# Kernel tuning notes

Measured on AMD Instinct MI355X. Metric: run time of the kernel, lower is better.

The kernel has to match this reference:

```python
import jax, jax.numpy as jnp
import numpy as np

N, F, H, C = 50000, 128, 4, 32  # nodes, in-features, heads, per-head dim
E = 800000
D = H * C  # concat output dim = 128


def _tconv(x, src, dst, ea, Wq, bq, Wk, bk, Wv, bv, We, Ws, bs):
    # PyG TransformerConv (concat=True, root_weight=True, beta=False, eval mode)
    n = x.shape[0]
    q = (x @ Wq + bq).reshape(n, H, C)
    k = (x @ Wk + bk).reshape(n, H, C)
    v = (x @ Wv + bv).reshape(n, H, C)
    e = (ea @ We).reshape(-1, H, C)            # edge embedding [E,H,C]
    kj = k[src] + e                            # gathered keys + edge emb
    alpha = jnp.einsum('ehc,ehc->eh', q[dst], kj) / jnp.sqrt(jnp.float32(C))
    amax = jax.ops.segment_max(alpha, dst, num_segments=n)
    ex = jnp.exp(alpha - amax[dst])
    denom = jax.ops.segment_sum(ex, dst, num_segments=n)
    w = ex / (denom[dst] + 1e-16)              # segment softmax over in-edges
    msg = (v[src] + e) * w[:, :, None]
    out = jax.ops.segment_sum(msg, dst, num_segments=n).reshape(n, D)
    return out + x @ Ws + bs                   # skip connection


def setup_inputs() -> dict:
    key = jax.random.key(0)
    ks = jax.random.split(key, 24)
    s = lambda i, shape, scale: jax.random.normal(ks[i], shape, dtype=jnp.float32) * scale
    inp = {
        'x': s(0, (N, F), 1.0),
        'edge_index': jax.random.randint(ks[1], (2, E), 0, N),
        'edge_attr': s(2, (E,), 1.0),
        # layer 1 (in = F)
        'Wq1': s(3, (F, D), 1.0 / np.sqrt(F)), 'bq1': jnp.zeros((D,), jnp.float32),
        'Wk1': s(4, (F, D), 1.0 / np.sqrt(F)), 'bk1': jnp.zeros((D,), jnp.float32),
        'Wv1': s(5, (F, D), 1.0 / np.sqrt(F)), 'bv1': jnp.zeros((D,), jnp.float32),
        'We1': s(6, (1, D), 1.0),
        'Ws1': s(7, (F, D), 1.0 / np.sqrt(F)), 'bs1': jnp.zeros((D,), jnp.float32),
        # layer 2 (in = D)
        'Wq2': s(8, (D, D), 1.0 / np.sqrt(D)), 'bq2': jnp.zeros((D,), jnp.float32),
        'Wk2': s(9, (D, D), 1.0 / np.sqrt(D)), 'bk2': jnp.zeros((D,), jnp.float32),
        'Wv2': s(10, (D, D), 1.0 / np.sqrt(D)), 'bv2': jnp.zeros((D,), jnp.float32),
        'We2': s(11, (1, D), 1.0),
        'Ws2': s(12, (D, D), 1.0 / np.sqrt(D)), 'bs2': jnp.zeros((D,), jnp.float32),
    }
    return inp


def reference(x, edge_index, edge_attr,
              Wq1, bq1, Wk1, bk1, Wv1, bv1, We1, Ws1, bs1,
              Wq2, bq2, Wk2, bk2, Wv2, bv2, We2, Ws2, bs2):
    src, dst = edge_index[0], edge_index[1]
    ea = edge_attr.reshape(-1, 1)
    h = _tconv(x, src, dst, ea, Wq1, bq1, Wk1, bk1, Wv1, bv1, We1, Ws1, bs1)
    h = jax.nn.relu(h)  # dropout is identity in eval mode
    h = _tconv(h, src, dst, ea, Wq2, bq2, Wk2, bk2, Wv2, bv2, We2, Ws2, bs2)
    return jax.nn.relu(h)
```

## Files before the change

### kernel.cpp

```cpp
#include <hip/hip_runtime.h>


#define TPB 256

typedef __attribute__((ext_vector_type(8))) short short8v;
typedef __attribute__((ext_vector_type(8))) unsigned short ushort8v;
typedef __attribute__((ext_vector_type(16))) float f32x16;

__device__ __forceinline__ unsigned short f2bf(float f) {
    unsigned u = __float_as_uint(f);
    u = (u + 0x7FFFu + ((u >> 16) & 1u)) >> 16;
    return (unsigned short)u;
}
__device__ __forceinline__ float bf2f(unsigned short s) {
    return __uint_as_float((unsigned)s << 16);
}
__device__ __forceinline__ float exp2_hw(float x) {
    float r;
    asm("v_exp_f32 %0, %1" : "=v"(r) : "v"(x));
    return r;
}

__device__ __forceinline__ void gemm_body(
    int idx, int nrt,
    const unsigned short* __restrict__ A, int M,
    const unsigned short* __restrict__ pack,
    const float* __restrict__ bq, const float* __restrict__ bk,
    const float* __restrict__ bv, const float* __restrict__ bs,
    unsigned short* __restrict__ oq, unsigned short* __restrict__ okv,
    unsigned short* __restrict__ os)
{
    if (idx >= nrt * 4) return;
    const int g = idx & 3;
    const int row0 = (idx >> 2) * 128;

    const int wv = threadIdx.x >> 6;
    const int lane = threadIdx.x & 63;
    const int rbase = row0 + wv * 32;
    const int arow = rbase + (lane & 31);
    const int kh = (lane >> 5) * 8;

    const short8v z8 = {0, 0, 0, 0, 0, 0, 0, 0};
    short8v a[8];
    if (arow < M) {
        const unsigned short* Ap = A + (size_t)arow * 128 + kh;
#pragma unroll
        for (int t = 0; t < 8; ++t) a[t] = *(const short8v*)(Ap + t * 16);
    } else {
#pragma unroll
        for (int t = 0; t < 8; ++t) a[t] = z8;
    }

    f32x16 acc[4];
#pragma unroll
    for (int nc = 0; nc < 4; ++nc)
#pragma unroll
        for (int r = 0; r < 16; ++r) acc[nc][r] = 0.f;

    const unsigned short* bp = pack + (size_t)g * 16384;
#pragma unroll
    for (int nc = 0; nc < 4; ++nc) {
#pragma unroll
        for (int t = 0; t < 8; ++t) {
            short8v b = *(const short8v*)(bp + (nc * 8 + t) * 512 + lane * 8);
            acc[nc] = __builtin_amdgcn_mfma_f32_32x32x16_bf16(a[t], b, acc[nc], 0, 0, 0);
        }
    }

    const float* bias = g == 0 ? bq : (g == 1 ? bk : (g == 2 ? bv : bs));
    const int col = lane & 31;
    const int rb2 = rbase + 4 * (lane >> 5);
    unsigned short* out = g == 0 ? oq : (g == 3 ? os : okv);
    const int stride = (g == 1 || g == 2) ? 256 : 128;
    const int goff = g == 2 ? 128 : 0;
#pragma unroll
    for (int nc = 0; nc < 4; ++nc) {
        float bb = bias[nc * 32 + col];
#pragma unroll
        for (int r = 0; r < 16; ++r) {
            int row = rb2 + (r & 3) + 8 * (r >> 2);
            if (row < M)
                out[(size_t)row * stride + goff + nc * 32 + col] = f2bf(acc[nc][r] + bb);
        }
    }
}

__device__ __forceinline__ void scatter_body(
    int sb, const int* __restrict__ src, const int* __restrict__ dst,
    const float* __restrict__ ea, const int* __restrict__ row_ptr,
    const int* __restrict__ edge_rank,
    unsigned* __restrict__ csr_pack, int E)
{
    const int base = (sb * TPB + threadIdx.x) * 4;
    if (base + 3 < E) {
        int4 d4 = *(const int4*)(dst + base);
        int4 s4 = *(const int4*)(src + base);
        float4 a4 = *(const float4*)(ea + base);
        int4 r4 = *(const int4*)(edge_rank + base);
        csr_pack[row_ptr[d4.x] + r4.x] = ((unsigned)f2bf(a4.x) << 16) | (unsigned)s4.x;
        csr_pack[row_ptr[d4.y] + r4.y] = ((unsigned)f2bf(a4.y) << 16) | (unsigned)s4.y;
        csr_pack[row_ptr[d4.z] + r4.z] = ((unsigned)f2bf(a4.z) << 16) | (unsigned)s4.z;
        csr_pack[row_ptr[d4.w] + r4.w] = ((unsigned)f2bf(a4.w) << 16) | (unsigned)s4.w;
    } else {
        for (int e = base; e < E; ++e) {
            csr_pack[row_ptr[dst[e]] + edge_rank[e]] =
                ((unsigned)f2bf(ea[e]) << 16) | (unsigned)src[e];
        }
    }
}

__global__ void __launch_bounds__(TPB) hist_prep_cvt_k(
    const int* __restrict__ dst, int* __restrict__ deg,
    int* __restrict__ edge_rank, int E, int gE4,
    const float* __restrict__ Wq1, const float* __restrict__ Wk1,
    const float* __restrict__ Wv1, const float* __restrict__ Ws1,
    const float* __restrict__ Wq2, const float* __restrict__ Wk2,
    const float* __restrict__ Wv2, const float* __restrict__ Ws2,
    unsigned short* __restrict__ pack,
    const float* __restrict__ x, unsigned short* __restrict__ xb, int n4)
{
    if (blockIdx.x < (unsigned)gE4) {
        const int base = (blockIdx.x * TPB + threadIdx.x) * 4;
        if (base + 3 < E) {
            int4 d4 = *(const int4*)(dst + base);
            int4 r4;
            r4.x = atomicAdd(&deg[d4.x], 1);
            r4.y = atomicAdd(&deg[d4.y], 1);
            r4.z = atomicAdd(&deg[d4.z], 1);
            r4.w = atomicAdd(&deg[d4.w], 1);
            *(int4*)(edge_rank + base) = r4;
        } else {
            for (int e = base; e < E; ++e)
                edge_rank[e] = atomicAdd(&deg[dst[e]], 1);
        }
    } else if (blockIdx.x < (unsigned)(gE4 + 512)) {
        int i = (blockIdx.x - gE4) * TPB + threadIdx.x;
        int j = i & 7, lane = (i >> 3) & 63, t = (i >> 9) & 7, nc = (i >> 12) & 3, g = (i >> 14) & 7;
        const float* Wt[8] = {Wq1, Wk1, Wv1, Ws1, Wq2, Wk2, Wv2, Ws2};
        const float* W = Wt[g];
        int kk = t * 16 + (lane >> 5) * 8 + j;
        int nn = nc * 32 + (lane & 31);
        pack[i] = f2bf(W[kk * 128 + nn]);
    } else {
        int i = (blockIdx.x - gE4 - 512) * TPB + threadIdx.x;
        if (i >= n4) return;
        float4 v = *(const float4*)(x + (size_t)i * 4);
        ushort4 o;
        o.x = f2bf(v.x); o.y = f2bf(v.y); o.z = f2bf(v.z); o.w = f2bf(v.w);
        *(ushort4*)(xb + (size_t)i * 4) = o;
    }
}

__global__ void __launch_bounds__(TPB) scan_a_k(const int* __restrict__ deg, int n,
                                                int* __restrict__ incl,
                                                int* __restrict__ bsum,
                                                int* __restrict__ bcnt, int nb,
                                                int* __restrict__ rank)
{
    __shared__ int ts[TPB];
    __shared__ int lhist[64];
    if (threadIdx.x < 64) lhist[threadIdx.x] = 0;
    const int base = blockIdx.x * 1024;
    int vals[4], s = 0;
#pragma unroll
    for (int j = 0; j < 4; ++j) {
        int i = base + threadIdx.x * 4 + j;
        vals[j] = (i < n) ? deg[i] : 0;
        s += vals[j];
    }
    ts[threadIdx.x] = s;
    __syncthreads();
#pragma unroll
    for (int j = 0; j < 4; ++j) {
        int i = base + threadIdx.x * 4 + j;
        if (i < n) {
            int bin = 63 - min(vals[j], 63);
            rank[i] = atomicAdd(&lhist[bin], 1);
        }
    }
    for (int off = 1; off < TPB; off <<= 1) {
        int u = (threadIdx.x >= off) ? ts[threadIdx.x - off] : 0;
        __syncthreads();
        ts[threadIdx.x] += u;
        __syncthreads();
    }
    int run = ts[threadIdx.x] - s;
#pragma unroll
    for (int j = 0; j < 4; ++j) {
        run += vals[j];
        int i = base + threadIdx.x * 4 + j;
        if (i < n) incl[i] = run;
    }
    if (threadIdx.x == TPB - 1) bsum[blockIdx.x] = ts[TPB - 1];
    __syncthreads();
    if (threadIdx.x < 64) bcnt[threadIdx.x * nb + blockIdx.x] = lhist[threadIdx.x];
}

__global__ void __launch_bounds__(TPB) scan_b_k(int* __restrict__ bsum, int nb,
                                                int* __restrict__ bcnt)
{
    __shared__ int ts[TPB];
    const int t = threadIdx.x;
    int v = (t < nb) ? bsum[t] : 0;
    ts[t] = v;
    __syncthreads();
    for (int off = 1; off < TPB; off <<= 1) {
        int u = (t >= off) ? ts[t - off] : 0;
        __syncthreads();
        ts[t] += u;
        __syncthreads();
    }
    if (t < nb) bsum[t] = ts[t] - v;
    __syncthreads();

    const int total = 64 * nb;
    const int C = (total + TPB - 1) / TPB;
    int loc[32];
    int s = 0;
    for (int j = 0; j < C; ++j) {
        int i = t * C + j;
        loc[j] = (i < total) ? bcnt[i] : 0;
        s += loc[j];
    }
    __syncthreads();
    ts[t] = s;
    __syncthreads();
    for (int off = 1; off < TPB; off <<= 1) {
        int u = (t >= off) ? ts[t - off] : 0;
        __syncthreads();
        ts[t] += u;
        __syncthreads();
    }
    int run = ts[t] - s;
    for (int j = 0; j < C; ++j) {
        int i = t * C + j;
        if (i < total) bcnt[i] = run;
        run += loc[j];
    }
}

__global__ void __launch_bounds__(TPB) finalize_k(const int* __restrict__ incl,
                                                  const int* __restrict__ deg,
                                                  const int* __restrict__ bsum, int n,
                                                  int* __restrict__ row_ptr,
                                                  const int* __restrict__ bcnt, int nb,
                                                  const int* __restrict__ rank,
                                                  int* __restrict__ perm)
{
    const int base = blockIdx.x * 1024;
    const int boff = bsum[blockIdx.x];
#pragma unroll
    for (int j = 0; j < 4; ++j) {
        int i = base + threadIdx.x * 4 + j;
        if (i < n) {
            int dg = deg[i];
            int iv = incl[i] + boff;
            row_ptr[i] = iv - dg;
            if (i == n - 1) row_ptr[n] = iv;
            int bin = 63 - min(dg, 63);
            perm[bcnt[bin * nb + blockIdx.x] + rank[i]] = i;
        }
    }
}

__global__ void __launch_bounds__(TPB) scatter_gemm_k(
    const int* __restrict__ src, const int* __restrict__ dst,
    const float* __restrict__ ea, const int* __restrict__ row_ptr,
    const int* __restrict__ edge_rank,
    unsigned* __restrict__ csr_pack, int E, int nSc,
    int nrt,
    const unsigned short* __restrict__ A, int M,
    const unsigned short* __restrict__ pack,
    const float* __restrict__ bq, const float* __restrict__ bk,
    const float* __restrict__ bv, const float* __restrict__ bs,
    unsigned short* __restrict__ oq, unsigned short* __restrict__ okv,
    unsigned short* __restrict__ os)
{
    const int b = blockIdx.x;
    const int n3 = b / 3, r = b - n3 * 3;
    if (b < 3 * nSc) {
        if (r == 2) scatter_body(n3, src, dst, ea, row_ptr, edge_rank, csr_pack, E);
        else gemm_body(2 * n3 + r, nrt, A, M, pack, bq, bk, bv, bs, oq, okv, os);
    } else {
        gemm_body(2 * nSc + (b - 3 * nSc), nrt, A, M, pack, bq, bk, bv, bs,
                  oq, okv, os);
    }
}

__global__ void __launch_bounds__(TPB) gemm_k(
    int nrt,
    const unsigned short* __restrict__ A, int M,
    const unsigned short* __restrict__ pack,
    const float* __restrict__ bq, const float* __restrict__ bk,
    const float* __restrict__ bv, const float* __restrict__ bs,
    unsigned short* __restrict__ oq, unsigned short* __restrict__ okv,
    unsigned short* __restrict__ os)
{
    gemm_body(blockIdx.x, nrt, A, M, pack, bq, bk, bv, bs, oq, okv, os);
}

template <bool BF16OUT>
__global__ void __launch_bounds__(TPB) node_attn_k(
    const unsigned short* __restrict__ q, const unsigned short* __restrict__ kv,
    const unsigned short* __restrict__ skip, const float* __restrict__ We,
    const int* __restrict__ row_ptr, const unsigned* __restrict__ csr_pack,
    const int* __restrict__ perm,
    void* __restrict__ outp, int n)
{
    const int slot = blockIdx.x * 16 + (threadIdx.x >> 4);
    if (slot >= n) return;
    const int node = perm[slot];
    const int l16 = threadIdx.x & 15;
    const int c8 = l16 * 8;

    const float C2 = 0.17677669529663687f * 1.44269504088896f;

    float we8[8], qv[8];
    {
        float4 wlo = *(const float4*)(We + c8);
        float4 whi = *(const float4*)(We + c8 + 4);
        we8[0] = wlo.x; we8[1] = wlo.y; we8[2] = wlo.z; we8[3] = wlo.w;
        we8[4] = whi.x; we8[5] = whi.y; we8[6] = whi.z; we8[7] = whi.w;
        ushort8v qu = *(const ushort8v*)(q + (size_t)node * 128 + c8);
#pragma unroll
        for (int i = 0; i < 8; ++i) qv[i] = bf2f((unsigned short)qu[i]) * C2;
    }

    float qwe = 0.f;
#pragma unroll
    for (int i = 0; i < 8; ++i) qwe = fmaf(qv[i], we8[i], qwe);
    qwe += __shfl_xor(qwe, 1);
    qwe += __shfl_xor(qwe, 2);

    const int p0 = row_ptr[node], p1 = row_ptr[node + 1];

    float m = -3.4e38f, l = 0.f, sae = 0.f;
    float acc[8];
#pragma unroll
    for (int i = 0; i < 8; ++i) acc[i] = 0.f;

    for (int j = p0; j < p1; j += 8) {
        const int last = p1 - 1;
        unsigned pr[8];
#pragma unroll
        for (int t = 0; t < 8; ++t) pr[t] = csr_pack[min(j + t, last)];

        ushort8v ku[8], vu[8];
#pragma unroll
        for (int t = 0; t < 8; ++t) {
            const unsigned short* b = kv + (pr[t] & 0xFFFFu) * 256u + c8;
            ku[t] = *(const ushort8v*)b;
            vu[t] = *(const ushort8v*)(b + 128);
        }

        float d[8];
#pragma unroll
        for (int t = 0; t < 8; ++t) {
            float dd = 0.f;
#pragma unroll
            for (int i = 0; i < 8; ++i)
                dd = fmaf(bf2f((unsigned short)ku[t][i]), qv[i], dd);
            dd += __shfl_xor(dd, 1);
            dd += __shfl_xor(dd, 2);
            d[t] = dd;
        }

        float eav[8], al[8];
#pragma unroll
        for (int t = 0; t < 8; ++t) {
            eav[t] = bf2f((unsigned short)(pr[t] >> 16));
            al[t] = (t == 0 || j + t < p1) ? fmaf(eav[t], qwe, d[t]) : -3.4e38f;
        }

        float mn = m;
#pragma unroll
        for (int t = 0; t < 8; ++t) mn = fmaxf(mn, al[t]);
        float sc = exp2_hw(m - mn);
        float pe[8];
#pragma unroll
        for (int t = 0; t < 8; ++t) pe[t] = exp2_hw(al[t] - mn);

        float ls = 0.f, ss = 0.f;
#pragma unroll
        for (int t = 0; t < 8; ++t) { ls += pe[t]; ss = fmaf(pe[t], eav[t], ss); }
        l = fmaf(l, sc, ls);
        sae = fmaf(sae, sc, ss);
#pragma unroll
        for (int i = 0; i < 8; ++i) {
            float mv = 0.f;
#pragma unroll
            for (int t = 0; t < 8; ++t)
                mv = fmaf(pe[t], bf2f((unsigned short)vu[t][i]), mv);
            acc[i] = fmaf(acc[i], sc, mv);
        }
        m = mn;
    }

    float inv = 1.f / (l + 1e-16f);
    ushort8v sku = *(const ushort8v*)(skip + (size_t)node * 128 + c8);
    float o[8];
#pragma unroll
    for (int i = 0; i < 8; ++i)
        o[i] = fmaxf(fmaf(fmaf(sae, we8[i], acc[i]), inv,
                          bf2f((unsigned short)sku[i])), 0.f);

    if (BF16OUT) {
        ushort8v ov;
#pragma unroll
        for (int i = 0; i < 8; ++i) ov[i] = f2bf(o[i]);
        *(ushort8v*)((unsigned short*)outp + (size_t)node * 128 + c8) = ov;
    } else {
        float* op = (float*)outp + (size_t)node * 128 + c8;
        *(float4*)op = make_float4(o[0], o[1], o[2], o[3]);
        *(float4*)(op + 4) = make_float4(o[4], o[5], o[6], o[7]);
    }
}

extern "C" void kernel_launch(void* const* d_in, const int* in_sizes, int n_in,
                              void* d_out, int out_size, void* d_ws, size_t ws_size,
                              hipStream_t stream)
{
    const float* x   = (const float*)d_in[0];
    const int*   ei  = (const int*)d_in[1];
    const float* ea  = (const float*)d_in[2];
    const float* Wq1 = (const float*)d_in[3];  const float* bq1 = (const float*)d_in[4];
    const float* Wk1 = (const float*)d_in[5];  const float* bk1 = (const float*)d_in[6];
    const float* Wv1 = (const float*)d_in[7];  const float* bv1 = (const float*)d_in[8];
    const float* We1 = (const float*)d_in[9];
    const float* Ws1 = (const float*)d_in[10]; const float* bs1 = (const float*)d_in[11];
    const float* Wq2 = (const float*)d_in[12]; const float* bq2 = (const float*)d_in[13];
    const float* Wk2 = (const float*)d_in[14]; const float* bk2 = (const float*)d_in[15];
    const float* Wv2 = (const float*)d_in[16]; const float* bv2 = (const float*)d_in[17];
    const float* We2 = (const float*)d_in[18];
    const float* Ws2 = (const float*)d_in[19]; const float* bs2 = (const float*)d_in[20];

    const int N = in_sizes[0] / 128;
    const int E = in_sizes[1] / 2;
    const int* src = ei;
    const int* dst = ei + E;
    float* outf = (float*)d_out;

    const int nb = (N + 1023) / 1024;

    unsigned short* q  = (unsigned short*)d_ws;
    unsigned short* kv = q + (size_t)N * 128;
    unsigned short* s  = kv + (size_t)N * 256;
    unsigned short* xb = s + (size_t)N * 128;
    unsigned short* pk = xb + (size_t)N * 128;
    int*   row_ptr = (int*)(pk + 131072);
    int*   deg     = row_ptr + (N + 1);
    int*   incl    = deg + N;
    int*   rank    = incl + N;
    int*   bsum    = rank + N;
    int*   bcnt    = bsum + 256;
    int*   perm    = bcnt + 64 * nb;
    int*   edge_rank = perm + N;
    unsigned* csr_pack = (unsigned*)(edge_rank + E);

    const int gN16 = (N + 15) / 16;
    const int n4   = N * 128 / 4;
    const int gCv  = (n4 + TPB - 1) / TPB;
    const int gE4  = (E + 1023) / 1024;
    const int nrt  = (N + 127) / 128;
    const int nGm  = nrt * 4;
    const int nSc  = gE4;

    hipMemsetAsync(deg, 0, (size_t)N * sizeof(int), stream);
    hist_prep_cvt_k<<<gE4 + 512 + gCv, TPB, 0, stream>>>(
        dst, deg, edge_rank, E, gE4,
        Wq1, Wk1, Wv1, Ws1, Wq2, Wk2, Wv2, Ws2, pk, x, xb, n4);
    scan_a_k<<<nb, TPB, 0, stream>>>(deg, N, incl, bsum, bcnt, nb, rank);
    scan_b_k<<<1, TPB, 0, stream>>>(bsum, nb, bcnt);
    finalize_k<<<nb, TPB, 0, stream>>>(incl, deg, bsum, N, row_ptr,
                                       bcnt, nb, rank, perm);
    scatter_gemm_k<<<nSc + nGm, TPB, 0, stream>>>(
        src, dst, ea, row_ptr, edge_rank, csr_pack, E, nSc, nrt,
        xb, N, pk, bq1, bk1, bv1, bs1, q, kv, s);
    node_attn_k<true><<<gN16, TPB, 0, stream>>>(q, kv, s, We1, row_ptr, csr_pack,
                                                perm, xb, N);
    gemm_k<<<nGm, TPB, 0, stream>>>(nrt, xb, N, pk + 65536,
                                    bq2, bk2, bv2, bs2, q, kv, s);
    node_attn_k<false><<<gN16, TPB, 0, stream>>>(q, kv, s, We2, row_ptr, csr_pack,
                                                 perm, outf, N);
}
```

Baseline: 263.3 us.

## Merge three-kernel CSR scan and degree bucketing into one single-block kernel

Replaces the multi-block scan, block-sum scan and finalize kernels with a single 768-thread block that computes row_ptr and a degree-bucketed node permutation using per-thread shared-memory histograms. This removes two kernel launches and the global intermediate arrays (incl, rank, bsum, bcnt). The trade-off is that one block now does serial work over all 50k nodes with strided, uncoalesced reads. It also cuts the degree buckets from 64 to 32 and uses 16-bit shared counters, which limits N to 65535 nodes.

```diff
diff --git a/kernel.cpp b/kernel.cpp
--- a/kernel.cpp
+++ b/kernel.cpp
@@ -2,6 +2,7 @@
 
 
 #define TPB 256
+#define SCT 768
 
 typedef __attribute__((ext_vector_type(8))) short short8v;
 typedef __attribute__((ext_vector_type(8))) unsigned short ushort8v;
@@ -151,114 +152,75 @@
     }
 }
 
-__global__ void __launch_bounds__(TPB) scan_a_k(const int* __restrict__ deg, int n,
-                                                int* __restrict__ incl,
-                                                int* __restrict__ bsum,
-                                                int* __restrict__ bcnt, int nb,
-                                                int* __restrict__ rank)
-{
-    __shared__ int ts[TPB];
-    __shared__ int lhist[64];
-    if (threadIdx.x < 64) lhist[threadIdx.x] = 0;
-    const int base = blockIdx.x * 1024;
-    int vals[4], s = 0;
-#pragma unroll
-    for (int j = 0; j < 4; ++j) {
-        int i = base + threadIdx.x * 4 + j;
-        vals[j] = (i < n) ? deg[i] : 0;
-        s += vals[j];
-    }
-    ts[threadIdx.x] = s;
+__global__ void __launch_bounds__(SCT) csr_scan_k(
+    const int* __restrict__ deg, int n,
+    int* __restrict__ row_ptr, int* __restrict__ perm)
+{
+    __shared__ unsigned short cnt[32 * SCT];
+    __shared__ int ts[SCT];
+    const int t = threadIdx.x;
+    const int C = (n + SCT - 1) / SCT;
+
+#pragma unroll
+    for (int b = 0; b < 32; ++b) cnt[b * SCT + t] = 0;
+
+    int s = 0;
+    for (int j = 0; j < C; ++j) {
+        int i = t * C + j;
+        if (i < n) {
+            int d = deg[i];
+            s += d;
+            cnt[(31 - min(d, 31)) * SCT + t]++;
+        }
+    }
+    ts[t] = s;
     __syncthreads();
-#pragma unroll
-    for (int j = 0; j < 4; ++j) {
-        int i = base + threadIdx.x * 4 + j;
-        if (i < n) {
-            int bin = 63 - min(vals[j], 63);
-            rank[i] = atomicAdd(&lhist[bin], 1);
-        }
-    }
-    for (int off = 1; off < TPB; off <<= 1) {
-        int u = (threadIdx.x >= off) ? ts[threadIdx.x - off] : 0;
-        __syncthreads();
-        ts[threadIdx.x] += u;
-        __syncthreads();
-    }
-    int run = ts[threadIdx.x] - s;
-#pragma unroll
-    for (int j = 0; j < 4; ++j) {
-        run += vals[j];
-        int i = base + threadIdx.x * 4 + j;
-        if (i < n) incl[i] = run;
-    }
-    if (threadIdx.x == TPB - 1) bsum[blockIdx.x] = ts[TPB - 1];
-    __syncthreads();
-    if (threadIdx.x < 64) bcnt[threadIdx.x * nb + blockIdx.x] = lhist[threadIdx.x];
-}
-
-__global__ void __launch_bounds__(TPB) scan_b_k(int* __restrict__ bsum, int nb,
-                                                int* __restrict__ bcnt)
-{
-    __shared__ int ts[TPB];
-    const int t = threadIdx.x;
-    int v = (t < nb) ? bsum[t] : 0;
-    ts[t] = v;
-    __syncthreads();
-    for (int off = 1; off < TPB; off <<= 1) {
+    for (int off = 1; off < SCT; off <<= 1) {
         int u = (t >= off) ? ts[t - off] : 0;
         __syncthreads();
         ts[t] += u;
         __syncthreads();
     }
-    if (t < nb) bsum[t] = ts[t] - v;
-    __syncthreads();
-
-    const int total = 64 * nb;
-    const int C = (total + TPB - 1) / TPB;
-    int loc[32];
-    int s = 0;
+    int run = ts[t] - s;
     for (int j = 0; j < C; ++j) {
         int i = t * C + j;
-        loc[j] = (i < total) ? bcnt[i] : 0;
-        s += loc[j];
+        if (i < n) {
+            row_ptr[i] = run;
+            run += deg[i];
+            if (i == n - 1) row_ptr[n] = run;
+        }
     }
     __syncthreads();
-    ts[t] = s;
+
+    int s2 = 0;
+    const int base2 = t * 32;
+#pragma unroll
+    for (int j = 0; j < 32; ++j) {
+        int v = cnt[base2 + j];
+        cnt[base2 + j] = (unsigned short)s2;
+        s2 += v;
+    }
+    ts[t] = s2;
     __syncthreads();
-    for (int off = 1; off < TPB; off <<= 1) {
+    for (int off = 1; off < SCT; off <<= 1) {
         int u = (t >= off) ? ts[t - off] : 0;
         __syncthreads();
         ts[t] += u;
         __syncthreads();
     }
-    int run = ts[t] - s;
+    int cb = ts[t] - s2;
+#pragma unroll
+    for (int j = 0; j < 32; ++j)
+        cnt[base2 + j] = (unsigned short)(cnt[base2 + j] + cb);
+    __syncthreads();
+
     for (int j = 0; j < C; ++j) {
         int i = t * C + j;
-        if (i < total) bcnt[i] = run;
-        run += loc[j];
-    }
-}
-
-__global__ void __launch_bounds__(TPB) finalize_k(const int* __restrict__ incl,
-                                                  const int* __restrict__ deg,
-                                                  const int* __restrict__ bsum, int n,
-                                                  int* __restrict__ row_ptr,
-                                                  const int* __restrict__ bcnt, int nb,
-                                                  const int* __restrict__ rank,
-                                                  int* __restrict__ perm)
-{
-    const int base = blockIdx.x * 1024;
-    const int boff = bsum[blockIdx.x];
-#pragma unroll
-    for (int j = 0; j < 4; ++j) {
-        int i = base + threadIdx.x * 4 + j;
         if (i < n) {
-            int dg = deg[i];
-            int iv = incl[i] + boff;
-            row_ptr[i] = iv - dg;
-            if (i == n - 1) row_ptr[n] = iv;
-            int bin = 63 - min(dg, 63);
-            perm[bcnt[bin * nb + blockIdx.x] + rank[i]] = i;
+            int b = 31 - min(deg[i], 31);
+            int p = cnt[b * SCT + t];
+            cnt[b * SCT + t] = (unsigned short)(p + 1);
+            perm[p] = i;
         }
     }
 }
@@ -440,8 +402,6 @@
     const int* dst = ei + E;
     float* outf = (float*)d_out;
 
-    const int nb = (N + 1023) / 1024;
-
     unsigned short* q  = (unsigned short*)d_ws;
     unsigned short* kv = q + (size_t)N * 128;
     unsigned short* s  = kv + (size_t)N * 256;
@@ -449,11 +409,7 @@
     unsigned short* pk = xb + (size_t)N * 128;
     int*   row_ptr = (int*)(pk + 131072);
     int*   deg     = row_ptr + (N + 1);
-    int*   incl    = deg + N;
-    int*   rank    = incl + N;
-    int*   bsum    = rank + N;
-    int*   bcnt    = bsum + 256;
-    int*   perm    = bcnt + 64 * nb;
+    int*   perm    = deg + N;
     int*   edge_rank = perm + N;
     unsigned* csr_pack = (unsigned*)(edge_rank + E);
 
@@ -469,10 +425,7 @@
     hist_prep_cvt_k<<<gE4 + 512 + gCv, TPB, 0, stream>>>(
         dst, deg, edge_rank, E, gE4,
         Wq1, Wk1, Wv1, Ws1, Wq2, Wk2, Wv2, Ws2, pk, x, xb, n4);
-    scan_a_k<<<nb, TPB, 0, stream>>>(deg, N, incl, bsum, bcnt, nb, rank);
-    scan_b_k<<<1, TPB, 0, stream>>>(bsum, nb, bcnt);
-    finalize_k<<<nb, TPB, 0, stream>>>(incl, deg, bsum, N, row_ptr,
-                                       bcnt, nb, rank, perm);
+    csr_scan_k<<<1, SCT, 0, stream>>>(deg, N, row_ptr, perm);
     scatter_gemm_k<<<nSc + nGm, TPB, 0, stream>>>(
         src, dst, ea, row_ptr, edge_rank, csr_pack, E, nSc, nrt,
         xb, N, pk, bq1, bk1, bv1, bs1, q, kv, s);
```

After: 406.1 us. +54.2%, slower.
